# Kernel optimization log

Measured on AMD Instinct MI355X. Metric: run time of the kernel, lower is better.

The kernel has to match this reference:

```python
import jax, jax.numpy as jnp
import numpy as np

T, C, NH, NL, NP = 5, 192, 4, 5, 4
DH = C // NH

def leaky(x):
    return jnp.where(x >= 0, x, 0.1 * x)

def conv2d(x, w, b, padding=1, dilation=1):
    out = jax.lax.conv_general_dilated(
        x, w, window_strides=(1, 1),
        padding=[(padding, padding), (padding, padding)],
        rhs_dilation=(dilation, dilation),
        dimension_numbers=('NCHW', 'OIHW', 'NCHW'))
    return out + b[None, :, None, None]

def grid_sample_border(img, gx, gy):
    # align_corners=True, padding_mode='border'; gx/gy normalized [-1,1], shape (B,H,W)
    B, Cc, H, W = img.shape
    x = jnp.clip((gx + 1.0) * 0.5 * (W - 1), 0.0, W - 1)
    y = jnp.clip((gy + 1.0) * 0.5 * (H - 1), 0.0, H - 1)
    x0 = jnp.floor(x); y0 = jnp.floor(y)
    wx = (x - x0).reshape(B, 1, -1); wy = (y - y0).reshape(B, 1, -1)
    flat = img.reshape(B, Cc, H * W)
    def g(yi, xi):
        xi = jnp.clip(xi, 0, W - 1).astype(jnp.int32)
        yi = jnp.clip(yi, 0, H - 1).astype(jnp.int32)
        return jnp.take_along_axis(flat, (yi * W + xi).reshape(B, 1, -1), axis=2)
    out = (g(y0, x0) * (1 - wx) * (1 - wy) + g(y0, x0 + 1) * wx * (1 - wy)
         + g(y0 + 1, x0) * (1 - wx) * wy + g(y0 + 1, x0 + 1) * wx * wy)
    return out.reshape(B, Cc, H, W)

def warp(x, flo):
    B, _, H, W = x.shape
    xx = jnp.arange(W, dtype=jnp.float32)[None, :] * jnp.ones((H, 1), jnp.float32)
    yy = jnp.arange(H, dtype=jnp.float32)[:, None] * jnp.ones((1, W), jnp.float32)
    gx = 2.0 * (xx[None] + flo[:, 0]) / max(W - 1, 1) - 1.0
    gy = 2.0 * (yy[None] + flo[:, 1]) / max(H - 1, 1) - 1.0
    return grid_sample_border(x, gx, gy)

def deform_sample(v_img, loc):
    # v_img (N,D,H,W); loc (N,Q,P,2) in [0,1]; bilinear, zeros padding, align_corners=False
    N, D, H, W = v_img.shape
    Q, P = loc.shape[1], loc.shape[2]
    x = loc[..., 0] * W - 0.5
    y = loc[..., 1] * H - 0.5
    x0 = jnp.floor(x); y0 = jnp.floor(y)
    wx = (x - x0).reshape(N, 1, -1); wy = (y - y0).reshape(N, 1, -1)
    flat = v_img.reshape(N, D, H * W)
    def g(yi, xi):
        valid = ((xi >= 0) & (xi <= W - 1) & (yi >= 0) & (yi <= H - 1)).astype(v_img.dtype)
        xi_c = jnp.clip(xi, 0, W - 1).astype(jnp.int32)
        yi_c = jnp.clip(yi, 0, H - 1).astype(jnp.int32)
        return jnp.take_along_axis(flat, (yi_c * W + xi_c).reshape(N, 1, -1), axis=2) * valid.reshape(N, 1, -1)
    out = (g(y0, x0) * (1 - wx) * (1 - wy) + g(y0, x0 + 1) * wx * (1 - wy)
         + g(y0 + 1, x0) * (1 - wx) * wy + g(y0 + 1, x0 + 1) * wx * wy)
    return out.reshape(N, D, Q, P)

def _forward(frame, srcframe, flow_forward, flow_backward,
             w_qk, b_qk, w_v, b_v, w_vproj, b_vproj, w_off, b_off,
             w_attn, b_attn, w_out, b_out, w_ff, b_ff,
             w_ffn1, b_ffn1, w_ffn2, b_ffn2):
    b, t, c, h, w = frame.shape
    ff01, ff12 = flow_forward[:, 0], flow_forward[:, 1]
    fb32, fb43 = flow_backward[:, 2], flow_backward[:, 3]
    ff02 = ff01 + warp(ff12, ff01)
    fb42 = fb43 + warp(fb32, fb43)
    warp02 = warp(frame[:, 0], ff02)
    warp12 = warp(frame[:, 1], ff12)
    warp32 = warp(frame[:, 3], fb32)
    warp42 = warp(frame[:, 4], fb42)
    qk_in = jnp.concatenate([warp02, warp12, frame[:, 2], warp32, warp42,
                             flow_forward.reshape(b, -1, h, w),
                             flow_backward.reshape(b, -1, h, w)], axis=1)
    queries = leaky(conv2d(qk_in, w_qk, b_qk)).reshape(b, t, c, h, w)
    value = leaky(conv2d(frame.reshape(b, t * c, h, w), w_v, b_v)).reshape(b, t, c, h, w)

    Lq = t * h * w
    q_tok = queries.transpose(0, 1, 3, 4, 2).reshape(b, Lq, c)
    v_tok = value.transpose(0, 1, 3, 4, 2).reshape(b, Lq, c)
    v_proj = (v_tok @ w_vproj.T + b_vproj).reshape(b, t, h * w, NH, DH)

    offs = (q_tok @ w_off.T + b_off).reshape(b, Lq, NH, NL, NP, 2)
    aw = (q_tok @ w_attn.T + b_attn).reshape(b, Lq, NH, NL * NP)
    aw = jax.nn.softmax(aw, axis=-1).reshape(b, Lq, NH, NL, NP)

    # reference points (all valid ratios are ones): ((x+0.5)/W, (y+0.5)/H)
    rx = (jnp.arange(w, dtype=frame.dtype) + 0.5) / w
    ry = (jnp.arange(h, dtype=frame.dtype) + 0.5) / h
    ref = jnp.stack(jnp.meshgrid(rx, ry, indexing='xy'), axis=-1).reshape(h * w, 2)
    ref = jnp.tile(ref, (t, 1))  # (Lq, 2)

    norm = jnp.array([w, h], dtype=frame.dtype)
    # flow-guided per-level displacement toward the center frame (level 2)
    zero = jnp.zeros_like(ff12)
    flows = jnp.stack([ff02, ff12, zero, fb32, fb42], axis=1)  # (b,NL,2,h,w)
    flow_norm = (flows / norm[None, None, :, None, None]).transpose(0, 1, 3, 4, 2).reshape(b, NL, h * w, 2)
    flow_norm = jnp.tile(flow_norm.transpose(0, 2, 1, 3), (1, t, 1, 1))  # (b,Lq,NL,2)

    loc = (ref[None, :, None, None, None, :]
           + offs / norm[None, None, None, None, None, :]
           + flow_norm[:, :, None, :, None, :])  # (b,Lq,NH,NL,NP,2)

    acc = jnp.zeros((b * NH, DH, Lq), dtype=frame.dtype)
    for l in range(NL):
        v_l = v_proj[:, l].transpose(0, 2, 3, 1).reshape(b * NH, DH, h, w)
        loc_l = loc[:, :, :, l].transpose(0, 2, 1, 3, 4).reshape(b * NH, Lq, NP, 2)
        samp = deform_sample(v_l, loc_l)  # (b*NH, DH, Lq, NP)
        w_l = aw[:, :, :, l].transpose(0, 2, 1, 3).reshape(b * NH, 1, Lq, NP)
        acc = acc + (samp * w_l).sum(-1)
    attn = acc.reshape(b, NH, DH, Lq).transpose(0, 3, 1, 2).reshape(b, Lq, c)
    attn = attn @ w_out.T + b_out

    out = attn.reshape(b, t, h, w, c).transpose(0, 1, 4, 2, 3).reshape(b * t, c, h, w)
    out = conv2d(out, w_ff, b_ff)
    out = out.reshape(b, t, c, h, w) + frame
    seq_in = jnp.concatenate([out.reshape(b * t, c, h, w), srcframe.reshape(b * t, c, h, w)], axis=1)
    ffn = conv2d(seq_in, w_ffn1, b_ffn1, padding=2, dilation=2)
    ffn = conv2d(leaky(ffn), w_ffn2, b_ffn2)
    out = out.reshape(b * t, c, h, w) + ffn
    return out.reshape(b, t, c, h, w)

def setup_inputs():
    key = jax.random.key(0)
    ks = jax.random.split(key, 16)
    B, H, W = 2, 64, 64
    s = 0.02
    d = {}
    d['frame'] = jax.random.normal(ks[0], (B, T, C, H, W), jnp.float32)
    d['srcframe'] = jax.random.normal(ks[1], (B, T, C, H, W), jnp.float32)
    d['flow_forward'] = jax.random.normal(ks[2], (B, 4, 2, H, W), jnp.float32)
    d['flow_backward'] = jax.random.normal(ks[3], (B, 4, 2, H, W), jnp.float32)
    cin_qk = T * C + 4 * (T - 1)
    d['w_qk'] = jax.random.normal(ks[4], (T * C, cin_qk, 3, 3), jnp.float32) * s
    d['b_qk'] = jnp.zeros((T * C,), jnp.float32)
    d['w_v'] = jax.random.normal(ks[5], (T * C, T * C, 3, 3), jnp.float32) * s
    d['b_v'] = jnp.zeros((T * C,), jnp.float32)
    d['w_vproj'] = jax.random.normal(ks[6], (C, C), jnp.float32) * s
    d['b_vproj'] = jnp.zeros((C,), jnp.float32)
    d['w_off'] = jax.random.normal(ks[7], (NH * NL * NP * 2, C), jnp.float32) * s
    d['b_off'] = jax.random.normal(ks[8], (NH * NL * NP * 2,), jnp.float32)
    d['w_attn'] = jax.random.normal(ks[9], (NH * NL * NP, C), jnp.float32) * s
    d['b_attn'] = jnp.zeros((NH * NL * NP,), jnp.float32)
    d['w_out'] = jax.random.normal(ks[10], (C, C), jnp.float32) * s
    d['b_out'] = jnp.zeros((C,), jnp.float32)
    d['w_ff'] = jax.random.normal(ks[11], (C, C, 3, 3), jnp.float32) * s
    d['b_ff'] = jnp.zeros((C,), jnp.float32)
    d['w_ffn1'] = jax.random.normal(ks[12], (C, 2 * C, 3, 3), jnp.float32) * s
    d['b_ffn1'] = jnp.zeros((C,), jnp.float32)
    d['w_ffn2'] = jax.random.normal(ks[13], (C, C, 3, 3), jnp.float32) * s
    d['b_ffn2'] = jnp.zeros((C,), jnp.float32)
    return d

def reference(frame, srcframe, flow_forward, flow_backward, w_qk, b_qk, w_v, b_v, w_vproj, b_vproj, w_off, b_off, w_attn, b_attn, w_out, b_out, w_ff, b_ff, w_ffn1, b_ffn1, w_ffn2, b_ffn2):
    out = _forward(frame, srcframe, flow_forward, flow_backward, w_qk, b_qk, w_v, b_v, w_vproj, b_vproj, w_off, b_off, w_attn, b_attn, w_out, b_out, w_ff, b_ff, w_ffn1, b_ffn1, w_ffn2, b_ffn2)
    return (out, srcframe)
```

## Files before the change

kernel.cpp:

```cpp
#include <hip/hip_runtime.h>


#define HWPX 4096
#define PPXN 4624
#define LQ   20480

typedef __attribute__((ext_vector_type(8))) short  short8;
typedef __attribute__((ext_vector_type(4))) short  short4v;
typedef __attribute__((ext_vector_type(4))) float  f32x4;

__device__ __forceinline__ unsigned short f2bf(float f) {
    unsigned u = __float_as_uint(f);
    unsigned r = (u + 0x7FFF + ((u >> 16) & 1)) >> 16;
    return (unsigned short)r;
}
__device__ __forceinline__ float bf2f(unsigned short s) {
    return __uint_as_float(((unsigned)s) << 16);
}

__device__ __forceinline__ void gl_lds16(const unsigned short* g, unsigned short* l) {
    __builtin_amdgcn_global_load_lds(
        (const __attribute__((address_space(1))) unsigned int*)g,
        (__attribute__((address_space(3))) unsigned int*)l, 16, 0, 0);
}

__device__ __forceinline__ float bsample(const float* __restrict__ p, float sx, float sy) {
    sx = fminf(fmaxf(sx, 0.f), 63.f);
    sy = fminf(fmaxf(sy, 0.f), 63.f);
    float x0 = floorf(sx), y0 = floorf(sy);
    int ix0 = (int)x0, iy0 = (int)y0;
    int ix1 = ix0 < 63 ? ix0 + 1 : 63;
    int iy1 = iy0 < 63 ? iy0 + 1 : 63;
    float wx = sx - x0, wy = sy - y0;
    float v00 = p[iy0*64+ix0], v01 = p[iy0*64+ix1];
    float v10 = p[iy1*64+ix0], v11 = p[iy1*64+ix1];
    return (v00*(1.f-wx) + v01*wx)*(1.f-wy) + (v10*(1.f-wx) + v11*wx)*wy;
}

__global__ __launch_bounds__(256) void k_flow(const float* __restrict__ ff,
                                              const float* __restrict__ fb,
                                              float* __restrict__ flows) {
    int i = blockIdx.x*256 + threadIdx.x;
    int b = i >> 12, pix = i & 4095;
    int x = pix & 63, y = pix >> 6;
    const float* ff01 = ff + (size_t)(b*4+0)*2*HWPX;
    const float* ff12 = ff + (size_t)(b*4+1)*2*HWPX;
    const float* fb32 = fb + (size_t)(b*4+2)*2*HWPX;
    const float* fb43 = fb + (size_t)(b*4+3)*2*HWPX;
    float* F = flows + (size_t)b*5*2*HWPX;
    float ax = ff01[pix], ay = ff01[HWPX+pix];
    float sx = bsample(ff12,      (float)x+ax, (float)y+ay);
    float sy = bsample(ff12+HWPX, (float)x+ax, (float)y+ay);
    F[0*2*HWPX + pix]        = ax + sx;
    F[0*2*HWPX + HWPX + pix] = ay + sy;
    F[1*2*HWPX + pix]        = ff12[pix];
    F[1*2*HWPX + HWPX + pix] = ff12[HWPX+pix];
    F[2*2*HWPX + pix]        = 0.f;
    F[2*2*HWPX + HWPX + pix] = 0.f;
    F[3*2*HWPX + pix]        = fb32[pix];
    F[3*2*HWPX + HWPX + pix] = fb32[HWPX+pix];
    float bx = fb43[pix], by = fb43[HWPX+pix];
    float tx = bsample(fb32,      (float)x+bx, (float)y+by);
    float ty = bsample(fb32+HWPX, (float)x+bx, (float)y+by);
    F[4*2*HWPX + pix]        = bx + tx;
    F[4*2*HWPX + HWPX + pix] = by + ty;
}

__global__ void k_qkin(const float* __restrict__ frame, const float* __restrict__ ff,
                       const float* __restrict__ fb, const float* __restrict__ flows,
                       unsigned short* __restrict__ Pqk)
{
    int ppx = blockIdx.x*64 + threadIdx.x;
    if (ppx >= PPXN) return;
    int b = blockIdx.z;
    int c8 = (blockIdx.y*4 + threadIdx.y)*8;
    unsigned short* dst = Pqk + ((size_t)b*PPXN + ppx)*992 + c8;
    int py = ppx/68, pxc = ppx - py*68;
    short8 o = {};
    if (py >= 2 && py < 66 && pxc >= 2 && pxc < 66 && c8 < 976) {
        int y = py-2, x = pxc-2, pix = (y<<6)+x;
        if (c8 >= 960) {
            #pragma unroll
            for (int j = 0; j < 8; ++j) {
                int k = c8 - 960 + j;
                float v = (k < 8) ? ff[((size_t)b*8 + k)*HWPX + pix]
                                  : fb[((size_t)b*8 + k - 8)*HWPX + pix];
                o[j] = (short)f2bf(v);
            }
        } else {
            int slot = c8/192, cc = c8 - slot*192;
            const float* base = frame + ((size_t)(b*5 + slot)*192)*HWPX;
            if (slot == 2) {
                #pragma unroll
                for (int j = 0; j < 8; ++j)
                    o[j] = (short)f2bf(base[(size_t)(cc+j)*HWPX + pix]);
            } else {
                const float* F = flows + ((size_t)(b*5 + slot)*2)*HWPX;
                float sx = fminf(fmaxf((float)x + F[pix], 0.f), 63.f);
                float sy = fminf(fmaxf((float)y + F[HWPX + pix], 0.f), 63.f);
                float x0 = floorf(sx), y0 = floorf(sy);
                int ix0 = (int)x0, iy0 = (int)y0;
                int ix1 = ix0 < 63 ? ix0+1 : 63, iy1 = iy0 < 63 ? iy0+1 : 63;
                float wx = sx - x0, wy = sy - y0;
                float w00 = (1.f-wx)*(1.f-wy), w01 = wx*(1.f-wy);
                float w10 = (1.f-wx)*wy,       w11 = wx*wy;
                int i00 = iy0*64+ix0, i01 = iy0*64+ix1;
                int i10 = iy1*64+ix0, i11 = iy1*64+ix1;
                #pragma unroll
                for (int j = 0; j < 8; ++j) {
                    const float* p = base + (size_t)(cc+j)*HWPX;
                    o[j] = (short)f2bf(p[i00]*w00 + p[i01]*w01 + p[i10]*w10 + p[i11]*w11);
                }
            }
        }
    }
    *(short8*)dst = o;
}

__global__ void t_pad(const float* __restrict__ in, unsigned short* __restrict__ outb,
                      int CI, int PITCH, int COFF)
{
    int ppx = blockIdx.x*64 + threadIdx.x;
    if (ppx >= PPXN) return;
    int img = blockIdx.z;
    int c8 = (blockIdx.y*4 + threadIdx.y)*8;
    unsigned short* dst = outb + ((size_t)img*PPXN + ppx)*PITCH;
    int py = ppx/68, pxc = ppx - py*68;
    if (py < 2 || py >= 66 || pxc < 2 || pxc >= 66) {
        short8 z = {};
        *(short8*)(dst + c8) = z;
        if (COFF) *(short8*)(dst + COFF + c8) = z;
        return;
    }
    int pix = ((py-2)<<6) + (pxc-2);
    short8 o;
    #pragma unroll
    for (int j = 0; j < 8; ++j)
        o[j] = (short)f2bf(in[((size_t)img*CI + c8 + j)*HWPX + pix]);
    *(short8*)(dst + COFF + c8) = o;
}

__global__ __launch_bounds__(256) void t_zb(unsigned short* __restrict__ buf, int PITCH) {
    int id = blockIdx.x*256 + threadIdx.x;
    int perpx = PITCH >> 3;
    int ppx = id / perpx, c8 = (id - ppx*perpx) * 8;
    if (ppx >= PPXN) return;
    int py = ppx/68, pxc = ppx - py*68;
    if (py >= 2 && py < 66 && pxc >= 2 && pxc < 66) return;
    short8 z = {};
    *(short8*)(buf + ((size_t)blockIdx.y*PPXN + ppx)*PITCH + c8) = z;
}

__global__ __launch_bounds__(256) void t_wT(const float* __restrict__ w,
                                            unsigned short* __restrict__ wT,
                                            int CI, int NKB) {
    int cotile = blockIdx.x, kblk = blockIdx.y;
    int tid = threadIdx.x & 255;
    unsigned short* dst = wT + ((size_t)(cotile*NKB + kblk))*18432;
    #pragma unroll
    for (int it = 0; it < 9; ++it) {
        int idx = it*256 + tid;
        int tap = idx >> 8, sub = idx & 255;
        int cg = sub >> 6, co = sub & 63;
        int cog = cotile*64 + co;
        int ci0 = kblk*32 + cg*8;
        short8 v;
        #pragma unroll
        for (int j = 0; j < 8; ++j) {
            int ci = ci0 + j;
            v[j] = (ci < CI) ? (short)f2bf(w[((size_t)cog*CI + ci)*9 + tap]) : (short)0;
        }
        *(short8*)(dst + (size_t)idx*8) = v;
    }
}

__global__ __launch_bounds__(256) void t_wg(const float* __restrict__ w1,
                                            const float* __restrict__ w2,
                                            unsigned short* __restrict__ wg,
                                            int co_split, int CO) {
    int cotile = blockIdx.x;
    int tid = threadIdx.x & 255;
    unsigned short* dst = wg + (size_t)cotile*12288;
    #pragma unroll
    for (int it = 0; it < 6; ++it) {
        int idx = it*256 + tid;
        int kblk = idx >> 8, sub = idx & 255;
        int cg = sub >> 6, co = sub & 63;
        int cog = cotile*64 + co;
        int ci0 = kblk*32 + cg*8;
        short8 v = {};
        if (cog < CO) {
            const float* row = (cog < co_split) ? w1 + (size_t)cog*192
                                                : w2 + (size_t)(cog - co_split)*192;
            #pragma unroll
            for (int j = 0; j < 8; ++j) v[j] = (short)f2bf(row[ci0 + j]);
        }
        *(short8*)(dst + (size_t)idx*8) = v;
    }
}

template<int DIL, int OMODE>
__global__ __launch_bounds__(256, 2) void k_conv(
    const unsigned short* __restrict__ P, int CIP, int NKB,
    const unsigned short* __restrict__ wT,
    const float* __restrict__ bias, const float* __restrict__ res,
    float* __restrict__ outF, unsigned short* __restrict__ outB, int CO)
{
    constexpr int RR    = 4 + 2*DIL;
    constexpr int XP    = 64 + 2*DIL;
    constexpr int PLANE = RR*XP*16;
    constexpr int NCH   = RR*XP*4;
    constexpr int NXS   = (NCH + 255)/256;
    __shared__ unsigned char  s_x[4*PLANE];
    __shared__ unsigned short s_w[18432];
    int tid = threadIdx.x & 255;
    int cotile = blockIdx.x, ytile = blockIdx.y, img = blockIdx.z;
    int y0 = ytile*4;
    const unsigned short* Pi = P + (size_t)img*PPXN*CIP;
    int w = tid >> 6, lane = tid & 63, lm = lane & 15, cig = lane >> 4;

    short8 xr[NXS];
    #pragma unroll
    for (int it = 0; it < NXS; ++it) {
        int li = it*256 + tid;
        if (li < NCH) {
            int p = li / (RR*XP), rem = li - p*(RR*XP);
            int r = rem / XP, col = rem - r*XP;
            xr[it] = *(const short8*)(Pi +
                ((size_t)((y0 + r + 2 - DIL)*68 + col + (2-DIL)))*CIP + p*8);
        }
    }
    {
        const unsigned short* ws = wT + ((size_t)cotile*NKB)*18432;
        #pragma unroll
        for (int it = 0; it < 9; ++it)
            gl_lds16(ws + (size_t)(it*256+tid)*8, &s_w[(it*256+tid)*8]);
    }
    #pragma unroll
    for (int it = 0; it < NXS; ++it) {
        int li = it*256 + tid;
        if (li < NCH) {
            int p = li / (RR*XP), rem = li - p*(RR*XP);
            *(short8*)&s_x[p*PLANE + rem*16] = xr[it];
        }
    }
    __syncthreads();

    f32x4 acc[4][4] = {};
    for (int kb = 0; kb < NKB; ++kb) {
        bool pf = (kb + 1 < NKB);
        if (pf) {
            int k0 = (kb+1)*32;
            #pragma unroll
            for (int it = 0; it < NXS; ++it) {
                int li = it*256 + tid;
                if (li < NCH) {
                    int p = li / (RR*XP), rem = li - p*(RR*XP);
                    int r = rem / XP, col = rem - r*XP;
                    xr[it] = *(const short8*)(Pi +
                        ((size_t)((y0 + r + 2 - DIL)*68 + col + (2-DIL)))*CIP + k0 + p*8);
                }
            }
        }
        #pragma unroll
        for (int t = 0; t < 9; ++t) {
            int ky = t/3, kx = t - ky*3;
            short8 A[4], Bf[4];
            #pragma unroll
            for (int nb = 0; nb < 4; ++nb)
                Bf[nb] = *(const short8*)&s_x[cig*PLANE +
                           ((w + ky*DIL)*XP + nb*16 + lm + kx*DIL)*16];
            #pragma unroll
            for (int mb = 0; mb < 4; ++mb)
                A[mb] = *(const short8*)&s_w[((t*4 + cig)*64 + mb*16 + lm)*8];
            #pragma unroll
            for (int mb = 0; mb < 4; ++mb)
                #pragma unroll
                for (int nb = 0; nb < 4; ++nb)
                    acc[mb][nb] = __builtin_amdgcn_mfma_f32_16x16x32_bf16(
                        A[mb], Bf[nb], acc[mb][nb], 0, 0, 0);
        }
        __syncthreads();
        if (pf) {
            const unsigned short* ws = wT + ((size_t)(cotile*NKB + kb + 1))*18432;
            #pragma unroll
            for (int it = 0; it < 9; ++it)
                gl_lds16(ws + (size_t)(it*256+tid)*8, &s_w[(it*256+tid)*8]);
            #pragma unroll
            for (int it = 0; it < NXS; ++it) {
                int li = it*256 + tid;
                if (li < NCH) {
                    int p = li / (RR*XP), rem = li - p*(RR*XP);
                    *(short8*)&s_x[p*PLANE + rem*16] = xr[it];
                }
            }
        }
        __syncthreads();
    }

    int y = y0 + w;
    #pragma unroll
    for (int mb = 0; mb < 4; ++mb) {
        int cob = cotile*64 + mb*16 + cig*4;
        #pragma unroll
        for (int nb = 0; nb < 4; ++nb) {
            int x = nb*16 + lm;
            int px = (y<<6) + x;
            float vv[4];
            #pragma unroll
            for (int r = 0; r < 4; ++r) {
                float v = acc[mb][nb][r] + bias[cob + r];
                if (OMODE == 0 || OMODE == 2) v = v >= 0.f ? v : 0.1f*v;
                if (OMODE == 1 || OMODE == 3)
                    v += res[((size_t)img*192 + cob + r)*HWPX + px];
                vv[r] = v;
            }
            if (OMODE == 0) {
                int it = cob/192, cc = cob - it*192;
                short4v s;
                #pragma unroll
                for (int r = 0; r < 4; ++r) s[r] = (short)f2bf(vv[r]);
                *(short4v*)(outB + (((size_t)(img*5 + it)*HWPX + px)*192 + cc)) = s;
            } else if (OMODE == 1) {
                #pragma unroll
                for (int r = 0; r < 4; ++r)
                    outF[((size_t)img*192 + cob + r)*HWPX + px] = vv[r];
                int ppx = ((px>>6)+2)*68 + (px&63) + 2;
                short4v s;
                #pragma unroll
                for (int r = 0; r < 4; ++r) s[r] = (short)f2bf(vv[r]);
                *(short4v*)(outB + ((size_t)img*PPXN + ppx)*384 + cob) = s;
            } else if (OMODE == 2) {
                int ppx = ((px>>6)+2)*68 + (px&63) + 2;
                short4v s;
                #pragma unroll
                for (int r = 0; r < 4; ++r) s[r] = (short)f2bf(vv[r]);
                *(short4v*)(outB + ((size_t)img*PPXN + ppx)*192 + cob) = s;
            } else {
                #pragma unroll
                for (int r = 0; r < 4; ++r)
                    outF[((size_t)img*192 + cob + r)*HWPX + px] = vv[r];
            }
        }
    }
}

template<int GMODE>
__global__ __launch_bounds__(256) void k_gemmm(
    const unsigned short* __restrict__ X, const unsigned short* __restrict__ WG,
    const float* __restrict__ b1, const float* __restrict__ b2,
    float* __restrict__ o1, float* __restrict__ o2, unsigned short* __restrict__ ob)
{
    __shared__ unsigned char  s_x[2][4*4096];
    __shared__ unsigned short s_w[12288];
    int tid = threadIdx.x & 255;
    int cotile = blockIdx.x, pxt = blockIdx.y, img = blockIdx.z;
    int px0 = pxt*256;
    const unsigned short* Xi = X + (size_t)img*HWPX*192;
    #pragma unroll
    for (int it = 0; it < 6; ++it)
        gl_lds16(WG + (size_t)cotile*12288 + (it*256+tid)*8, &s_w[(it*256+tid)*8]);
    short8 xr[4];
    #pragma unroll
    for (int it = 0; it < 4; ++it)
        xr[it] = *(const short8*)(Xi + (size_t)(px0 + tid)*192 + it*8);
    #pragma unroll
    for (int it = 0; it < 4; ++it)
        *(short8*)&s_x[0][it*4096 + tid*16] = xr[it];
    __syncthreads();
    int w = tid >> 6, lane = tid & 63, lm = lane & 15, cig = lane >> 4;
    f32x4 acc[4][4] = {};
    int xb = 0;
    for (int kb = 0; kb < 6; ++kb) {
        bool pf = (kb < 5);
        if (pf) {
            int k0 = (kb+1)*32;
            #pragma unroll
            for (int it = 0; it < 4; ++it)
                xr[it] = *(const short8*)(Xi + (size_t)(px0 + tid)*192 + k0 + it*8);
        }
        short8 A[4], Bf[4];
        #pragma unroll
        for (int nb = 0; nb < 4; ++nb)
            Bf[nb] = *(const short8*)&s_x[xb][cig*4096 + (w*64 + nb*16 + lm)*16];
        #pragma unroll
        for (int mb = 0; mb < 4; ++mb)
            A[mb] = *(const short8*)&s_w[((kb*4 + cig)*64 + mb*16 + lm)*8];
        #pragma unroll
        for (int mb = 0; mb < 4; ++mb)
            #pragma unroll
            for (int nb = 0; nb < 4; ++nb)
                acc[mb][nb] = __builtin_amdgcn_mfma_f32_16x16x32_bf16(
                    A[mb], Bf[nb], acc[mb][nb], 0, 0, 0);
        if (pf) {
            #pragma unroll
            for (int it = 0; it < 4; ++it)
                *(short8*)&s_x[xb^1][it*4096 + tid*16] = xr[it];
        }
        __syncthreads();
        xb ^= 1;
    }
    int b = img/5, t = img - b*5;
    #pragma unroll
    for (int mb = 0; mb < 4; ++mb) {
        int cob = cotile*64 + mb*16 + cig*4;
        if (GMODE == 1 && cob >= 240) continue;
        #pragma unroll
        for (int nb = 0; nb < 4; ++nb) {
            int px = px0 + w*64 + nb*16 + lm;
            float vv[4];
            #pragma unroll
            for (int r = 0; r < 4; ++r) {
                float bv;
                if (GMODE == 1) bv = (cob + r < 160) ? b1[cob+r] : b2[cob+r-160];
                else bv = b1[cob + r];
                vv[r] = acc[mb][nb][r] + bv;
            }
            if (GMODE == 0) {
                int h = cob/48, d = cob - h*48;
                short4v s;
                #pragma unroll
                for (int r = 0; r < 4; ++r) s[r] = (short)f2bf(vv[r]);
                *(short4v*)(ob + (((size_t)img*4 + h)*HWPX + px)*48 + d) = s;
            } else if (GMODE == 1) {
                #pragma unroll
                for (int r = 0; r < 4; ++r) {
                    int co = cob + r;
                    if (co < 160) o1[((size_t)b*160 + co)*LQ + t*HWPX + px] = vv[r];
                    else          o2[((size_t)b*80 + co-160)*LQ + t*HWPX + px] = vv[r];
                }
            } else {
                int ppx = ((px>>6)+2)*68 + (px&63) + 2;
                short4v s;
                #pragma unroll
                for (int r = 0; r < 4; ++r) s[r] = (short)f2bf(vv[r]);
                *(short4v*)(ob + ((size_t)img*PPXN + ppx)*192 + cob) = s;
            }
        }
    }
}

__global__ __launch_bounds__(256) void k_softmax20(float* __restrict__ aw) {
    int i = blockIdx.x*256 + threadIdx.x;
    int lq = i % LQ;
    int bh = i / LQ;
    float* p = aw + (size_t)bh*20*LQ + lq;
    float e[20];
    float m = -1e30f;
    #pragma unroll
    for (int j = 0; j < 20; ++j) { e[j] = p[(size_t)j*LQ]; m = fmaxf(m, e[j]); }
    float s = 0.f;
    #pragma unroll
    for (int j = 0; j < 20; ++j) { e[j] = expf(e[j]-m); s += e[j]; }
    float inv = 1.f/s;
    #pragma unroll
    for (int j = 0; j < 20; ++j) p[(size_t)j*LQ] = e[j]*inv;
}

__device__ __forceinline__ void addtap(float* acc, const unsigned short* __restrict__ src, float w) {
    const short8* s8 = (const short8*)src;
    #pragma unroll
    for (int q = 0; q < 6; ++q) {
        short8 v = s8[q];
        #pragma unroll
        for (int j = 0; j < 8; ++j)
            acc[q*8+j] += w * bf2f((unsigned short)v[j]);
    }
}

__global__ __launch_bounds__(256) void k_sample(
    const unsigned short* __restrict__ vp, const float* __restrict__ offs,
    const float* __restrict__ aw, const float* __restrict__ flows,
    unsigned short* __restrict__ accout)
{
    int blk = blockIdx.x;
    int b = blk / 320, sub = blk - b*320;
    int h = threadIdx.x >> 6;
    int lq = sub*64 + (threadIdx.x & 63);
    int pix = lq & 4095;
    int x = pix & 63, y = pix >> 6;
    const float* offp = offs + ((size_t)b*160 + h*40)*LQ + lq;
    const float* awp  = aw   + ((size_t)b*80  + h*20)*LQ + lq;
    float acc[48];
    #pragma unroll
    for (int d = 0; d < 48; ++d) acc[d] = 0.f;

    for (int l = 0; l < 5; ++l) {
        float fx = flows[((size_t)(b*5+l)*2+0)*HWPX + pix];
        float fy = flows[((size_t)(b*5+l)*2+1)*HWPX + pix];
        const unsigned short* vpl = vp + ((size_t)(b*5+l)*4 + h)*HWPX*48;
        #pragma unroll
        for (int p = 0; p < 4; ++p) {
            int o = l*4 + p;
            float ox = offp[(size_t)(2*o)*LQ];
            float oy = offp[(size_t)(2*o+1)*LQ];
            float wv = awp[(size_t)o*LQ];
            float sx = (float)x + ox + fx;
            float sy = (float)y + oy + fy;
            float x0f = floorf(sx), y0f = floorf(sy);
            float wx = sx - x0f, wy = sy - y0f;
            int ix0 = (int)x0f, iy0 = (int)y0f;
            float w00 = wv*(1.f-wx)*(1.f-wy), w01 = wv*wx*(1.f-wy);
            float w10 = wv*(1.f-wx)*wy,       w11 = wv*wx*wy;
            bool vx0 = (ix0 >= 0)  && (ix0 <= 63);
            bool vx1 = (ix0 >= -1) && (ix0 <= 62);
            bool vy0 = (iy0 >= 0)  && (iy0 <= 63);
            bool vy1 = (iy0 >= -1) && (iy0 <= 62);
            if (vy0 && vx0) addtap(acc, vpl + (size_t)(iy0*64 + ix0)*48,       w00);
            if (vy0 && vx1) addtap(acc, vpl + (size_t)(iy0*64 + ix0 + 1)*48,   w01);
            if (vy1 && vx0) addtap(acc, vpl + (size_t)((iy0+1)*64 + ix0)*48,   w10);
            if (vy1 && vx1) addtap(acc, vpl + (size_t)((iy0+1)*64 + ix0+1)*48, w11);
        }
    }
    unsigned short* dst = accout + ((size_t)b*LQ + lq)*192 + h*48;
    #pragma unroll
    for (int q = 0; q < 6; ++q) {
        short8 s;
        #pragma unroll
        for (int j = 0; j < 8; ++j) s[j] = (short)f2bf(acc[q*8+j]);
        *(short8*)(dst + q*8) = s;
    }
}


extern "C" void kernel_launch(void* const* d_in, const int* in_sizes, int n_in,
                              void* d_out, int out_size, void* d_ws, size_t ws_size,
                              hipStream_t stream) {
    (void)in_sizes; (void)n_in; (void)out_size; (void)ws_size;
    const float* frame    = (const float*)d_in[0];
    const float* srcframe = (const float*)d_in[1];
    const float* flow_f   = (const float*)d_in[2];
    const float* flow_b   = (const float*)d_in[3];
    const float* w_qk  = (const float*)d_in[4];  const float* b_qk  = (const float*)d_in[5];
    const float* w_v   = (const float*)d_in[6];  const float* b_v   = (const float*)d_in[7];
    const float* w_vp  = (const float*)d_in[8];  const float* b_vp  = (const float*)d_in[9];
    const float* w_off = (const float*)d_in[10]; const float* b_off = (const float*)d_in[11];
    const float* w_at  = (const float*)d_in[12]; const float* b_at  = (const float*)d_in[13];
    const float* w_out = (const float*)d_in[14]; const float* b_out = (const float*)d_in[15];
    const float* w_ff  = (const float*)d_in[16]; const float* b_ff  = (const float*)d_in[17];
    const float* w_f1  = (const float*)d_in[18]; const float* b_f1  = (const float*)d_in[19];
    const float* w_f2  = (const float*)d_in[20]; const float* b_f2  = (const float*)d_in[21];
    float* out = (float*)d_out;
    char* W = (char*)d_ws;

    float*          flows  = (float*)(W + 0);
    unsigned short* wT_qk  = (unsigned short*)(W + 327680);
    unsigned short* wT_v   = (unsigned short*)(W + 17469440);
    unsigned short* wT_ff  = (unsigned short*)(W + 327680);
    unsigned short* wT_f1  = (unsigned short*)(W + 991232);
    unsigned short* wT_f2  = (unsigned short*)(W + 2318336);
    unsigned short* wg_vp  = (unsigned short*)(W + 2981888);
    unsigned short* wg_oa  = (unsigned short*)(W + 3055616);
    unsigned short* wg_out = (unsigned short*)(W + 3153920);
    unsigned short* P_qk   = (unsigned short*)(W + 34058240);
    unsigned short* P_ff   = P_qk;
    unsigned short* P_v    = (unsigned short*)(W + 52406272);
    unsigned short* P_mid  = P_v;
    unsigned short* Q_tok  = (unsigned short*)(W + 70162432);
    unsigned short* acc_tok= Q_tok;
    unsigned short* V_tok  = (unsigned short*)(W + 85891072);
    unsigned short* P_ffn1 = V_tok;
    unsigned short* vp     = (unsigned short*)(W + 101619712);
    float*          offs   = (float*)(W + 121403392);
    float*          aw     = (float*)(W + 147617792);
    float*          out1   = (float*)(W + 160724992);

    dim3 bp(64, 4);

    k_flow<<<32, 256, 0, stream>>>(flow_f, flow_b, flows);
    t_wT<<<dim3(15,31), 256, 0, stream>>>(w_qk, wT_qk, 976, 31);
    t_wT<<<dim3(15,30), 256, 0, stream>>>(w_v,  wT_v,  960, 30);
    k_qkin<<<dim3(73,31,2), bp, 0, stream>>>(frame, flow_f, flow_b, flows, P_qk);
    t_pad<<<dim3(73,30,2), bp, 0, stream>>>(frame, P_v, 960, 960, 0);
    k_conv<1,0><<<dim3(15,16,2), 256, 0, stream>>>(P_qk, 992, 31, wT_qk, b_qk, nullptr,
                                                   nullptr, Q_tok, 960);
    k_conv<1,0><<<dim3(15,16,2), 256, 0, stream>>>(P_v, 960, 30, wT_v, b_v, nullptr,
                                                   nullptr, V_tok, 960);
    t_wT<<<dim3(3,6),  256, 0, stream>>>(w_ff, wT_ff, 192, 6);
    t_wT<<<dim3(3,12), 256, 0, stream>>>(w_f1, wT_f1, 384, 12);
    t_wT<<<dim3(3,6),  256, 0, stream>>>(w_f2, wT_f2, 192, 6);
    t_wg<<<3, 256, 0, stream>>>(w_vp,  nullptr, wg_vp, 192, 192);
    t_wg<<<4, 256, 0, stream>>>(w_off, w_at,    wg_oa, 160, 240);
    t_wg<<<3, 256, 0, stream>>>(w_out, nullptr, wg_out, 192, 192);
    t_zb<<<dim3(434,10), 256, 0, stream>>>(P_ff, 192);
    t_zb<<<dim3(434,10), 256, 0, stream>>>(P_mid, 192);
    k_gemmm<0><<<dim3(3,16,10), 256, 0, stream>>>(V_tok, wg_vp, b_vp, nullptr,
                                                  nullptr, nullptr, vp);
    k_gemmm<1><<<dim3(4,16,10), 256, 0, stream>>>(Q_tok, wg_oa, b_off, b_at,
                                                  offs, aw, nullptr);
    k_softmax20<<<640, 256, 0, stream>>>(aw);
    k_sample<<<640, 256, 0, stream>>>(vp, offs, aw, flows, acc_tok);
    t_pad<<<dim3(73,6,10), bp, 0, stream>>>(srcframe, P_ffn1, 192, 384, 192);
    k_gemmm<2><<<dim3(3,16,10), 256, 0, stream>>>(acc_tok, wg_out, b_out, nullptr,
                                                  nullptr, nullptr, P_ff);
    k_conv<1,1><<<dim3(3,16,10), 256, 0, stream>>>(P_ff, 192, 6, wT_ff, b_ff, frame,
                                                   out1, P_ffn1, 192);
    k_conv<2,2><<<dim3(3,16,10), 256, 0, stream>>>(P_ffn1, 384, 12, wT_f1, b_f1, nullptr,
                                                   nullptr, P_mid, 192);
    k_conv<1,3><<<dim3(3,16,10), 256, 0, stream>>>(P_mid, 192, 6, wT_f2, b_f2, out1,
                                                   out, nullptr, 192);
    hipMemcpyAsync(out + (size_t)2*5*192*HWPX, srcframe,
                   (size_t)2*5*192*HWPX*sizeof(float),
                   hipMemcpyDeviceToDevice, stream);
}
```

Measured before the change: 894.6 us.

## Double-buffer conv via direct LDS loads, merge QK/V convs, read padded bf16 in qkin

```diff
diff --git a/kernel.cpp b/kernel.cpp
--- a/kernel.cpp
+++ b/kernel.cpp
@@ -66,8 +66,9 @@
     F[4*2*HWPX + HWPX + pix] = by + ty;
 }
 
-__global__ void k_qkin(const float* __restrict__ frame, const float* __restrict__ ff,
-                       const float* __restrict__ fb, const float* __restrict__ flows,
+__global__ void k_qkin(const unsigned short* __restrict__ Pv,
+                       const float* __restrict__ ff, const float* __restrict__ fb,
+                       const float* __restrict__ flows,
                        unsigned short* __restrict__ Pqk)
 {
     int ppx = blockIdx.x*64 + threadIdx.x;
@@ -88,12 +89,10 @@
                 o[j] = (short)f2bf(v);
             }
         } else {
-            int slot = c8/192, cc = c8 - slot*192;
-            const float* base = frame + ((size_t)(b*5 + slot)*192)*HWPX;
+            const unsigned short* Pvb = Pv + (size_t)b*PPXN*960;
+            int slot = c8/192;
             if (slot == 2) {
-                #pragma unroll
-                for (int j = 0; j < 8; ++j)
-                    o[j] = (short)f2bf(base[(size_t)(cc+j)*HWPX + pix]);
+                o = *(const short8*)(Pvb + (size_t)ppx*960 + c8);
             } else {
                 const float* F = flows + ((size_t)(b*5 + slot)*2)*HWPX;
                 float sx = fminf(fmaxf((float)x + F[pix], 0.f), 63.f);
@@ -104,12 +103,15 @@
                 float wx = sx - x0, wy = sy - y0;
                 float w00 = (1.f-wx)*(1.f-wy), w01 = wx*(1.f-wy);
                 float w10 = (1.f-wx)*wy,       w11 = wx*wy;
-                int i00 = iy0*64+ix0, i01 = iy0*64+ix1;
-                int i10 = iy1*64+ix0, i11 = iy1*64+ix1;
+                short8 v00 = *(const short8*)(Pvb + ((size_t)((iy0+2)*68 + ix0+2))*960 + c8);
+                short8 v01 = *(const short8*)(Pvb + ((size_t)((iy0+2)*68 + ix1+2))*960 + c8);
+                short8 v10 = *(const short8*)(Pvb + ((size_t)((iy1+2)*68 + ix0+2))*960 + c8);
+                short8 v11 = *(const short8*)(Pvb + ((size_t)((iy1+2)*68 + ix1+2))*960 + c8);
                 #pragma unroll
                 for (int j = 0; j < 8; ++j) {
-                    const float* p = base + (size_t)(cc+j)*HWPX;
-                    o[j] = (short)f2bf(p[i00]*w00 + p[i01]*w01 + p[i10]*w10 + p[i11]*w11);
+                    float v = bf2f((unsigned short)v00[j])*w00 + bf2f((unsigned short)v01[j])*w01
+                            + bf2f((unsigned short)v10[j])*w10 + bf2f((unsigned short)v11[j])*w11;
+                    o[j] = (short)f2bf(v);
                 }
             }
         }
@@ -199,147 +201,138 @@
     }
 }
 
-template<int DIL, int OMODE>
-__global__ __launch_bounds__(256, 2) void k_conv(
-    const unsigned short* __restrict__ P, int CIP, int NKB,
-    const unsigned short* __restrict__ wT,
-    const float* __restrict__ bias, const float* __restrict__ res,
-    float* __restrict__ outF, unsigned short* __restrict__ outB, int CO)
+template<int ROWS, int DIL, int OMODE>
+__global__ __launch_bounds__(256) void k_conv(
+    const unsigned short* __restrict__ P0, const unsigned short* __restrict__ P1,
+    int CIP0, int CIP1, int NKB0, int NKB1,
+    const unsigned short* __restrict__ wT0, const unsigned short* __restrict__ wT1,
+    const float* __restrict__ bias0, const float* __restrict__ bias1,
+    const float* __restrict__ res, float* __restrict__ outF,
+    unsigned short* __restrict__ outB0, unsigned short* __restrict__ outB1,
+    int njobs, int CO)
 {
-    constexpr int RR    = 4 + 2*DIL;
+    constexpr int RR    = ROWS*4 + 2*DIL;
     constexpr int XP    = 64 + 2*DIL;
     constexpr int PLANE = RR*XP*16;
     constexpr int NCH   = RR*XP*4;
     constexpr int NXS   = (NCH + 255)/256;
-    __shared__ unsigned char  s_x[4*PLANE];
-    __shared__ unsigned short s_w[18432];
+    __shared__ unsigned char  s_x[2][4*PLANE];
+    __shared__ unsigned short s_w[2][18432];
+
     int tid = threadIdx.x & 255;
-    int cotile = blockIdx.x, ytile = blockIdx.y, img = blockIdx.z;
-    int y0 = ytile*4;
+    int cotile = blockIdx.x, ytile = blockIdx.y;
+    int z = blockIdx.z;
+    int sel = (njobs == 2) ? (z >> 1) : 0;
+    int img = (njobs == 2) ? (z & 1)  : z;
+    const unsigned short* P  = sel ? P1  : P0;
+    const unsigned short* wT = sel ? wT1 : wT0;
+    const float* bias        = sel ? bias1 : bias0;
+    unsigned short* outB     = sel ? outB1 : outB0;
+    int CIP = sel ? CIP1 : CIP0;
+    int NKB = sel ? NKB1 : NKB0;
+
+    int y0 = ytile * (ROWS*4);
     const unsigned short* Pi = P + (size_t)img*PPXN*CIP;
     int w = tid >> 6, lane = tid & 63, lm = lane & 15, cig = lane >> 4;
 
-    short8 xr[NXS];
-    #pragma unroll
-    for (int it = 0; it < NXS; ++it) {
-        int li = it*256 + tid;
-        if (li < NCH) {
-            int p = li / (RR*XP), rem = li - p*(RR*XP);
-            int r = rem / XP, col = rem - r*XP;
-            xr[it] = *(const short8*)(Pi +
-                ((size_t)((y0 + r + 2 - DIL)*68 + col + (2-DIL)))*CIP + p*8);
-        }
-    }
-    {
-        const unsigned short* ws = wT + ((size_t)cotile*NKB)*18432;
+    auto stage_x = [&](int kb, int buf) {
+        int k0 = kb*32;
+        #pragma unroll
+        for (int it = 0; it < NXS; ++it) {
+            int li = it*256 + tid;
+            if (li < NCH) {
+                int p = li / (RR*XP), rem = li - p*(RR*XP);
+                int r = rem / XP, c = rem - r*XP;
+                gl_lds16(Pi + ((size_t)((y0 + 2 - DIL + r)*68 + c + 2 - DIL))*CIP + k0 + p*8,
+                         (unsigned short*)&s_x[buf][li*16]);
+            }
+        }
+    };
+    auto stage_w = [&](int kb, int buf) {
+        const unsigned short* ws = wT + ((size_t)(cotile*NKB + kb))*18432;
         #pragma unroll
         for (int it = 0; it < 9; ++it)
-            gl_lds16(ws + (size_t)(it*256+tid)*8, &s_w[(it*256+tid)*8]);
-    }
-    #pragma unroll
-    for (int it = 0; it < NXS; ++it) {
-        int li = it*256 + tid;
-        if (li < NCH) {
-            int p = li / (RR*XP), rem = li - p*(RR*XP);
-            *(short8*)&s_x[p*PLANE + rem*16] = xr[it];
-        }
-    }
+            gl_lds16(ws + (size_t)(it*256+tid)*8, &s_w[buf][(it*256+tid)*8]);
+    };
+
+    stage_x(0, 0); stage_w(0, 0);
     __syncthreads();
 
-    f32x4 acc[4][4] = {};
+    f32x4 acc[4][ROWS*4] = {};
+    int buf = 0;
     for (int kb = 0; kb < NKB; ++kb) {
-        bool pf = (kb + 1 < NKB);
-        if (pf) {
-            int k0 = (kb+1)*32;
-            #pragma unroll
-            for (int it = 0; it < NXS; ++it) {
-                int li = it*256 + tid;
-                if (li < NCH) {
-                    int p = li / (RR*XP), rem = li - p*(RR*XP);
-                    int r = rem / XP, col = rem - r*XP;
-                    xr[it] = *(const short8*)(Pi +
-                        ((size_t)((y0 + r + 2 - DIL)*68 + col + (2-DIL)))*CIP + k0 + p*8);
-                }
-            }
-        }
+        if (kb + 1 < NKB) { stage_x(kb+1, buf^1); stage_w(kb+1, buf^1); }
         #pragma unroll
         for (int t = 0; t < 9; ++t) {
             int ky = t/3, kx = t - ky*3;
-            short8 A[4], Bf[4];
-            #pragma unroll
-            for (int nb = 0; nb < 4; ++nb)
-                Bf[nb] = *(const short8*)&s_x[cig*PLANE +
-                           ((w + ky*DIL)*XP + nb*16 + lm + kx*DIL)*16];
+            short8 A[4];
             #pragma unroll
             for (int mb = 0; mb < 4; ++mb)
-                A[mb] = *(const short8*)&s_w[((t*4 + cig)*64 + mb*16 + lm)*8];
-            #pragma unroll
-            for (int mb = 0; mb < 4; ++mb)
+                A[mb] = *(const short8*)&s_w[buf][((t*4 + cig)*64 + mb*16 + lm)*8];
+            #pragma unroll
+            for (int s = 0; s < ROWS; ++s) {
+                short8 Bf[4];
                 #pragma unroll
-                for (int nb = 0; nb < 4; ++nb)
-                    acc[mb][nb] = __builtin_amdgcn_mfma_f32_16x16x32_bf16(
-                        A[mb], Bf[nb], acc[mb][nb], 0, 0, 0);
+                for (int nc = 0; nc < 4; ++nc)
+                    Bf[nc] = *(const short8*)&s_x[buf][cig*PLANE +
+                               ((w*ROWS + s + ky*DIL)*XP + nc*16 + lm + kx*DIL)*16];
+                #pragma unroll
+                for (int mb = 0; mb < 4; ++mb)
+                    #pragma unroll
+                    for (int nc = 0; nc < 4; ++nc)
+                        acc[mb][s*4+nc] = __builtin_amdgcn_mfma_f32_16x16x32_bf16(
+                            A[mb], Bf[nc], acc[mb][s*4+nc], 0, 0, 0);
+            }
         }
         __syncthreads();
-        if (pf) {
-            const unsigned short* ws = wT + ((size_t)(cotile*NKB + kb + 1))*18432;
-            #pragma unroll
-            for (int it = 0; it < 9; ++it)
-                gl_lds16(ws + (size_t)(it*256+tid)*8, &s_w[(it*256+tid)*8]);
-            #pragma unroll
-            for (int it = 0; it < NXS; ++it) {
-                int li = it*256 + tid;
-                if (li < NCH) {
-                    int p = li / (RR*XP), rem = li - p*(RR*XP);
-                    *(short8*)&s_x[p*PLANE + rem*16] = xr[it];
-                }
-            }
-        }
-        __syncthreads();
-    }
-
-    int y = y0 + w;
+        buf ^= 1;
+    }
+
     #pragma unroll
     for (int mb = 0; mb < 4; ++mb) {
         int cob = cotile*64 + mb*16 + cig*4;
         #pragma unroll
-        for (int nb = 0; nb < 4; ++nb) {
-            int x = nb*16 + lm;
-            int px = (y<<6) + x;
-            float vv[4];
-            #pragma unroll
-            for (int r = 0; r < 4; ++r) {
-                float v = acc[mb][nb][r] + bias[cob + r];
-                if (OMODE == 0 || OMODE == 2) v = v >= 0.f ? v : 0.1f*v;
-                if (OMODE == 1 || OMODE == 3)
-                    v += res[((size_t)img*192 + cob + r)*HWPX + px];
-                vv[r] = v;
-            }
-            if (OMODE == 0) {
-                int it = cob/192, cc = cob - it*192;
-                short4v s;
+        for (int s = 0; s < ROWS; ++s) {
+            int y = y0 + w*ROWS + s;
+            #pragma unroll
+            for (int nc = 0; nc < 4; ++nc) {
+                int x = nc*16 + lm;
+                int px = (y<<6) + x;
+                float vv[4];
                 #pragma unroll
-                for (int r = 0; r < 4; ++r) s[r] = (short)f2bf(vv[r]);
-                *(short4v*)(outB + (((size_t)(img*5 + it)*HWPX + px)*192 + cc)) = s;
-            } else if (OMODE == 1) {
-                #pragma unroll
-                for (int r = 0; r < 4; ++r)
-                    outF[((size_t)img*192 + cob + r)*HWPX + px] = vv[r];
-                int ppx = ((px>>6)+2)*68 + (px&63) + 2;
-                short4v s;
-                #pragma unroll
-                for (int r = 0; r < 4; ++r) s[r] = (short)f2bf(vv[r]);
-                *(short4v*)(outB + ((size_t)img*PPXN + ppx)*384 + cob) = s;
-            } else if (OMODE == 2) {
-                int ppx = ((px>>6)+2)*68 + (px&63) + 2;
-                short4v s;
-                #pragma unroll
-                for (int r = 0; r < 4; ++r) s[r] = (short)f2bf(vv[r]);
-                *(short4v*)(outB + ((size_t)img*PPXN + ppx)*192 + cob) = s;
-            } else {
-                #pragma unroll
-                for (int r = 0; r < 4; ++r)
-                    outF[((size_t)img*192 + cob + r)*HWPX + px] = vv[r];
+                for (int r = 0; r < 4; ++r) {
+                    float v = acc[mb][s*4+nc][r] + bias[cob + r];
+                    if (OMODE == 0 || OMODE == 2) v = v >= 0.f ? v : 0.1f*v;
+                    if (OMODE == 1 || OMODE == 3)
+                        v += res[((size_t)img*192 + cob + r)*HWPX + px];
+                    vv[r] = v;
+                }
+                if (OMODE == 0) {
+                    int it = cob/192, cc = cob - it*192;
+                    short4v sv;
+                    #pragma unroll
+                    for (int r = 0; r < 4; ++r) sv[r] = (short)f2bf(vv[r]);
+                    *(short4v*)(outB + (((size_t)(img*5 + it)*HWPX + px)*192 + cc)) = sv;
+                } else if (OMODE == 1) {
+                    #pragma unroll
+                    for (int r = 0; r < 4; ++r)
+                        outF[((size_t)img*192 + cob + r)*HWPX + px] = vv[r];
+                    int ppx = ((px>>6)+2)*68 + (px&63) + 2;
+                    short4v sv;
+                    #pragma unroll
+                    for (int r = 0; r < 4; ++r) sv[r] = (short)f2bf(vv[r]);
+                    *(short4v*)(outB + ((size_t)img*PPXN + ppx)*384 + cob) = sv;
+                } else if (OMODE == 2) {
+                    int ppx = ((px>>6)+2)*68 + (px&63) + 2;
+                    short4v sv;
+                    #pragma unroll
+                    for (int r = 0; r < 4; ++r) sv[r] = (short)f2bf(vv[r]);
+                    *(short4v*)(outB + ((size_t)img*PPXN + ppx)*192 + cob) = sv;
+                } else {
+                    #pragma unroll
+                    for (int r = 0; r < 4; ++r)
+                        outF[((size_t)img*192 + cob + r)*HWPX + px] = vv[r];
+                }
             }
         }
     }
@@ -570,12 +563,11 @@
     k_flow<<<32, 256, 0, stream>>>(flow_f, flow_b, flows);
     t_wT<<<dim3(15,31), 256, 0, stream>>>(w_qk, wT_qk, 976, 31);
     t_wT<<<dim3(15,30), 256, 0, stream>>>(w_v,  wT_v,  960, 30);
-    k_qkin<<<dim3(73,31,2), bp, 0, stream>>>(frame, flow_f, flow_b, flows, P_qk);
     t_pad<<<dim3(73,30,2), bp, 0, stream>>>(frame, P_v, 960, 960, 0);
-    k_conv<1,0><<<dim3(15,16,2), 256, 0, stream>>>(P_qk, 992, 31, wT_qk, b_qk, nullptr,
-                                                   nullptr, Q_tok, 960);
-    k_conv<1,0><<<dim3(15,16,2), 256, 0, stream>>>(P_v, 960, 30, wT_v, b_v, nullptr,
-                                                   nullptr, V_tok, 960);
+    k_qkin<<<dim3(73,31,2), bp, 0, stream>>>(P_v, flow_f, flow_b, flows, P_qk);
+    k_conv<2,1,0><<<dim3(15,8,4), 256, 0, stream>>>(
+        P_qk, P_v, 992, 960, 31, 30, wT_qk, wT_v, b_qk, b_v,
+        nullptr, nullptr, Q_tok, V_tok, 2, 960);
     t_wT<<<dim3(3,6),  256, 0, stream>>>(w_ff, wT_ff, 192, 6);
     t_wT<<<dim3(3,12), 256, 0, stream>>>(w_f1, wT_f1, 384, 12);
     t_wT<<<dim3(3,6),  256, 0, stream>>>(w_f2, wT_f2, 192, 6);
@@ -593,12 +585,15 @@
     t_pad<<<dim3(73,6,10), bp, 0, stream>>>(srcframe, P_ffn1, 192, 384, 192);
     k_gemmm<2><<<dim3(3,16,10), 256, 0, stream>>>(acc_tok, wg_out, b_out, nullptr,
                                                   nullptr, nullptr, P_ff);
-    k_conv<1,1><<<dim3(3,16,10), 256, 0, stream>>>(P_ff, 192, 6, wT_ff, b_ff, frame,
-                                                   out1, P_ffn1, 192);
-    k_conv<2,2><<<dim3(3,16,10), 256, 0, stream>>>(P_ffn1, 384, 12, wT_f1, b_f1, nullptr,
-                                                   nullptr, P_mid, 192);
-    k_conv<1,3><<<dim3(3,16,10), 256, 0, stream>>>(P_mid, 192, 6, wT_f2, b_f2, out1,
-                                                   out, nullptr, 192);
+    k_conv<1,1,1><<<dim3(3,16,10), 256, 0, stream>>>(
+        P_ff, nullptr, 192, 0, 6, 0, wT_ff, nullptr, b_ff, nullptr,
+        frame, out1, P_ffn1, nullptr, 1, 192);
+    k_conv<1,2,2><<<dim3(3,16,10), 256, 0, stream>>>(
+        P_ffn1, nullptr, 384, 0, 12, 0, wT_f1, nullptr, b_f1, nullptr,
+        nullptr, nullptr, P_mid, nullptr, 1, 192);
+    k_conv<1,1,3><<<dim3(3,16,10), 256, 0, stream>>>(
+        P_mid, nullptr, 192, 0, 6, 0, wT_f2, nullptr, b_f2, nullptr,
+        out1, out, nullptr, nullptr, 1, 192);
     hipMemcpyAsync(out + (size_t)2*5*192*HWPX, srcframe,
                    (size_t)2*5*192*HWPX*sizeof(float),
                    hipMemcpyDeviceToDevice, stream);
```

After: 964.1 us. 7.8% more time.
